# Kernel optimization log

Measured on AMD Instinct MI355X. Metric: run time of the kernel, lower is better.

## Reference

```python
import jax, jax.numpy as jnp
import numpy as np

MIN_DECAY = 0.8
N_SAMPLES = 32768
N_FRAMES = 128
D = 128
BATCH = 128
N_EVENTS = 8
START = 8      # ConvUpsample start size
SLOPE = 0.2    # leaky_relu negative slope


def _tconv(x, w, b):
    # ConvTranspose1d(kernel=4, stride=2, padding=1) -> doubles length.
    # Equivalent dilated conv needs explicit padding k-1-p = 2 per side.
    y = jax.lax.conv_transpose(x, w, strides=(2,), padding=[(2, 2)],
                               dimension_numbers=('NCH', 'IOH', 'NCH'))
    return y + b[None, :, None]


def setup_inputs() -> dict:
    key = jax.random.key(0)
    ks = jax.random.split(key, 16)
    s = 0.1  # weight_init
    inp = {
        'x': jax.random.normal(ks[0], (BATCH, N_EVENTS, D), jnp.float32),
        'noise': jax.random.uniform(ks[1], (BATCH * N_EVENTS, 1, N_SAMPLES), jnp.float32, -10.0, 10.0),
        'Wup': jax.random.normal(ks[2], (D, D * START), jnp.float32) * s,
        'bup': jnp.zeros((D * START,), jnp.float32),
    }
    for i in range(3):
        inp[f'Wd{i}'] = jax.random.normal(ks[3 + i], (D, D), jnp.float32) * s
        inp[f'bd{i}'] = jnp.zeros((D,), jnp.float32)
    inp['Wdo'] = jax.random.normal(ks[6], (D, 1), jnp.float32) * s
    inp['bdo'] = jnp.zeros((1,), jnp.float32)
    chans = [D, D, D, D, 1]  # frames: 8->16->32->64->128, last layer to 1 channel
    for i in range(4):
        inp[f'Wc{i}'] = jax.random.normal(ks[7 + i], (chans[i], chans[i + 1], 4), jnp.float32) * s
        inp[f'bc{i}'] = jnp.zeros((chans[i + 1],), jnp.float32)
    return inp


def reference(x, noise, Wup, bup, Wd0, bd0, Wd1, bd1, Wd2, bd2, Wdo, bdo,
              Wc0, bc0, Wc1, bc1, Wc2, bc2, Wc3, bc3):
    B, E, Dm = x.shape
    xf = x.reshape(-1, Dm)                      # [BE, D]
    # decay head: LinearOutputStack(D, 3, out_channels=1)
    h = xf
    for W, b in ((Wd0, bd0), (Wd1, bd1), (Wd2, bd2)):
        h = jax.nn.leaky_relu(h @ W + b, SLOPE)
    decay = MIN_DECAY + jax.nn.sigmoid(h @ Wdo + bdo) * (1.0 - MIN_DECAY)  # [BE, 1]
    # ConvUpsample('learned'): linear -> [BE, D, 8] -> 4 doubling tconvs -> [BE, 1, F]
    u = (xf @ Wup + bup).reshape(-1, Dm, START)
    u = jax.nn.leaky_relu(_tconv(u, Wc0, bc0), SLOPE)
    u = jax.nn.leaky_relu(_tconv(u, Wc1, bc1), SLOPE)
    u = jax.nn.leaky_relu(_tconv(u, Wc2, bc2), SLOPE)
    u = _tconv(u, Wc3, bc3)                     # [BE, 1, F]
    u = u ** 2
    # exponential-decay recurrence: v[i] = u[i] + decay * v[i-1]
    def step(carry, ut):
        v = ut + decay * carry
        return v, v
    seq = jnp.moveaxis(u, -1, 0)                # [F, BE, 1]
    _, vs = jax.lax.scan(step, jnp.zeros_like(seq[0]), seq)
    v = jnp.moveaxis(vs, 0, -1)                 # [BE, 1, F]
    # linear interpolation F -> N_SAMPLES (align_corners=False)
    pos = (jnp.arange(N_SAMPLES) + 0.5) * (N_FRAMES / N_SAMPLES) - 0.5
    pos = jnp.clip(pos, 0.0, N_FRAMES - 1)
    i0 = jnp.floor(pos).astype(jnp.int32)
    i1 = jnp.minimum(i0 + 1, N_FRAMES - 1)
    w = (pos - i0).astype(v.dtype)
    out = v[..., i0] * (1.0 - w) + v[..., i1] * w  # [BE, 1, N]
    out = out * noise
    return out.reshape(B, E, 1, N_SAMPLES)
```

## Files before the change

kernel.cpp:

```cpp
#include <hip/hip_runtime.h>

#define SLOPE 0.2f
__device__ __forceinline__ float lrelu(float v){ return v > 0.0f ? v : SLOPE*v; }

template<int LT, int LF, int IS, int OS, bool RELU>
__device__ __forceinline__ void tconv_tile(const float* __restrict__ W,
                                           const float* __restrict__ bias,
                                           const float* __restrict__ in,
                                           int base,
                                           float* __restrict__ out,
                                           int obase,
                                           int co, int q)
{
  constexpr int TQ = LT/2;
  constexpr int NI = LT/4;
  const int i0 = base + q*NI;
  float acc[TQ];
  {
    const float b = bias[co];
    #pragma unroll
    for (int j=0;j<TQ;j++) acc[j]=b;
  }
  const bool hasM1 = (i0 > 0);
  const bool hasE  = (i0 + NI < LF);
  #pragma unroll 2
  for (int ci=0; ci<128; ci++){
    const float4 w = *(const float4*)(W + ((size_t)ci*128 + co)*4);
    const float* xin = in + ci*IS + i0;
    const float xm1 = hasM1 ? xin[-1] : 0.0f;
    const float xE  = hasE  ? xin[NI] : 0.0f;
    float xv[NI];
    if constexpr (NI==2){ const float2 t=*(const float2*)xin; xv[0]=t.x; xv[1]=t.y; }
    else { const float4 t=*(const float4*)xin;
      xv[0]=t.x; xv[1]=t.y; xv[2]=t.z; xv[3]=t.w; }
    acc[0]    += xm1*w.x;
    acc[TQ-1] += xE *w.w;
    #pragma unroll
    for (int li=0; li<NI; li++){
      const float x = xv[li];
      acc[2*li]   += x*w.z;
      acc[2*li+1] += x*w.y;
      if (li<NI-1) acc[2*li+2] += x*w.x;
      if (li>0)    acc[2*li-1] += x*w.w;
    }
  }
  float* op = out + co*OS + obase + q*TQ;
  #pragma unroll
  for (int j=0;j<TQ;j++) op[j] = RELU ? lrelu(acc[j]) : acc[j];
}

__device__ __forceinline__ void final_tile(const float* __restrict__ Wc3,
                                           const float* __restrict__ bc3,
                                           const float* __restrict__ bufC,
                                           float* __restrict__ part,
                                           float* __restrict__ fr,
                                           int tt, int c, int g, int tid)
{
  const int off = tt*32;
  const int t = c;
  const bool inwin = (tt==0) ? (t < 63) : (t >= 63);
  const bool even = ((t & 1) == 0);
  const int i  = t >> 1;
  const int ia = even ? (i-1) : i;
  const int ib = even ? i : (i+1);
  const int sa = ia - off + 1;
  const int sbr = ib - off + 1;
  const float mb = (sbr <= 32) ? 1.0f : 0.0f;
  const int sb = (sbr <= 32) ? sbr : 32;
  float a = 0.0f;
  if (inwin){
    const int cb = g*32;
    #pragma unroll 4
    for (int k=0;k<32;k++){
      const int ci = cb + k;
      const float4 w = *(const float4*)(Wc3 + (size_t)ci*4);
      const float wa = even ? w.x : w.y;
      const float wb = even ? w.z : w.w;
      a += bufC[ci*33 + sa]*wa + (bufC[ci*33 + sb]*mb)*wb;
    }
  }
  part[g*128 + t] = a;
  __syncthreads();
  if (tid < 128 && ((tt==0) ? (tid < 63) : (tid >= 63))){
    const float s = part[tid]+part[128+tid]+part[256+tid]+part[384+tid] + bc3[0];
    fr[tid] = s*s;
  }
}

extern "C" __global__ __launch_bounds__(512, 8)
void npg_compute(const float* __restrict__ x,
                 const float* __restrict__ noise,
                 const float* __restrict__ Wup, const float* __restrict__ bup,
                 const float* __restrict__ Wd0, const float* __restrict__ bd0,
                 const float* __restrict__ Wd1, const float* __restrict__ bd1,
                 const float* __restrict__ Wd2, const float* __restrict__ bd2,
                 const float* __restrict__ Wdo, const float* __restrict__ bdo,
                 const float* __restrict__ Wc0, const float* __restrict__ bc0,
                 const float* __restrict__ Wc1, const float* __restrict__ bc1,
                 const float* __restrict__ Wc2, const float* __restrict__ bc2,
                 const float* __restrict__ Wc3, const float* __restrict__ bc3,
                 float* __restrict__ outp)
{
  __shared__ float R0[128*32];
  __shared__ float R1[128*33];
  __shared__ float part[512];
  __shared__ float fr[128];
  __shared__ float sdecay;

  float* const xrow = R1;
  float* const h0   = R1 + 128;
  float* const h1   = R1 + 256;

  const int tid = threadIdx.x;
  const int row = blockIdx.x;
  const int c   = tid & 127;
  const int g   = tid >> 7;

  if (tid < 128) xrow[tid] = x[row*128 + tid];
  __syncthreads();

  {
    const float* inb = xrow;
    const float* Ws[3] = {Wd0, Wd1, Wd2};
    const float* bs[3] = {bd0, bd1, bd2};
    float* outs[3] = {h0, h1, h0};
    #pragma unroll
    for (int layer=0; layer<3; layer++){
      float a = 0.0f;
      const int base = g*32;
      const float* W = Ws[layer];
      #pragma unroll 8
      for (int i=0;i<32;i++) a += inb[base+i]*W[(size_t)(base+i)*128 + c];
      part[g*128 + c] = a;
      __syncthreads();
      if (tid < 128){
        const float v = part[tid]+part[128+tid]+part[256+tid]+part[384+tid] + bs[layer][tid];
        outs[layer][tid] = lrelu(v);
      }
      __syncthreads();
      inb = outs[layer];
    }
    if (tid < 128) part[tid] = h0[tid]*Wdo[tid];
    __syncthreads();
    if (tid < 64){
      float v = part[tid] + part[tid+64];
      #pragma unroll
      for (int off=32; off>0; off>>=1) v += __shfl_down(v, off, 64);
      if (tid==0){
        const float z = v + bdo[0];
        sdecay = 0.8f + 0.2f/(1.0f + expf(-z));
      }
    }
    __syncthreads();
  }

  {
    const int o = tid*2;
    float2 a = make_float2(bup[o], bup[o+1]);
    #pragma unroll 4
    for (int i=0;i<128;i++){
      const float xv = xrow[i];
      const float2 w = *(const float2*)(Wup + (size_t)i*1024 + o);
      a.x += xv*w.x; a.y += xv*w.y;
    }
    R0[o] = a.x; R0[o+1] = a.y;
    __syncthreads();
  }

  tconv_tile<8 , 8, 8, 16, true>(Wc0, bc0, R0, 0, R1, 0, c, g);  __syncthreads();
  tconv_tile<16,16,16, 32, true>(Wc1, bc1, R1, 0, R0, 0, c, g);  __syncthreads();

  tconv_tile<16,32,32, 33, true>(Wc2, bc2, R0, 0, R1, 1, c, g);
  if (tid < 128) R1[tid*33] = 0.0f;
  __syncthreads();

  final_tile(Wc3, bc3, R1, part, fr, 0, c, g, tid);
  if (tid >= 128 && tid < 256){
    const int ci = tid - 128;
    R1[ci*33] = R1[ci*33 + 32];
  }
  __syncthreads();

  tconv_tile<16,32,32, 33, true>(Wc2, bc2, R0, 16, R1, 1, c, g);
  __syncthreads();

  final_tile(Wc3, bc3, R1, part, fr, 1, c, g, tid);
  __syncthreads();

  {
    float d = sdecay;
    #pragma unroll
    for (int o=1;o<128;o<<=1){
      const float prev = (tid < 128 && tid >= o) ? fr[tid-o] : 0.0f;
      __syncthreads();
      if (tid < 128) fr[tid] += d*prev;
      __syncthreads();
      d = d*d;
    }
  }

  {
    const float4* __restrict__ nz4 = (const float4*)(noise + (size_t)row*32768);
    float4*       __restrict__ o4  = (float4*)(outp  + (size_t)row*32768);
    #pragma unroll 8
    for (int it=0; it<16; ++it){
      const int idx = it*512 + tid;
      const float4 nz = nz4[idx];
      const int n = idx*4;
      float r[4];
      #pragma unroll
      for (int j=0;j<4;j++){
        float pos = ((float)(n+j) + 0.5f) * (1.0f/256.0f) - 0.5f;
        pos = fminf(fmaxf(pos, 0.0f), 127.0f);
        const int i0 = (int)pos;
        const int i1 = min(i0+1, 127);
        const float w = pos - (float)i0;
        r[j] = fr[i0]*(1.0f-w) + fr[i1]*w;
      }
      float4 o;
      o.x = r[0]*nz.x; o.y = r[1]*nz.y; o.z = r[2]*nz.z; o.w = r[3]*nz.w;
      o4[idx] = o;
    }
  }
}

extern "C" void kernel_launch(void* const* d_in, const int* in_sizes, int n_in,
                              void* d_out, int out_size, void* d_ws, size_t ws_size,
                              hipStream_t stream)
{
  const float* x    = (const float*)d_in[0];
  const float* noise= (const float*)d_in[1];
  const float* Wup  = (const float*)d_in[2];
  const float* bup  = (const float*)d_in[3];
  const float* Wd0  = (const float*)d_in[4];
  const float* bd0  = (const float*)d_in[5];
  const float* Wd1  = (const float*)d_in[6];
  const float* bd1  = (const float*)d_in[7];
  const float* Wd2  = (const float*)d_in[8];
  const float* bd2  = (const float*)d_in[9];
  const float* Wdo  = (const float*)d_in[10];
  const float* bdo  = (const float*)d_in[11];
  const float* Wc0  = (const float*)d_in[12];
  const float* bc0  = (const float*)d_in[13];
  const float* Wc1  = (const float*)d_in[14];
  const float* bc1  = (const float*)d_in[15];
  const float* Wc2  = (const float*)d_in[16];
  const float* bc2  = (const float*)d_in[17];
  const float* Wc3  = (const float*)d_in[18];
  const float* bc3  = (const float*)d_in[19];
  float* out = (float*)d_out;

  hipLaunchKernelGGL(npg_compute, dim3(1024), dim3(512), 0, stream,
                     x, noise, Wup, bup, Wd0, bd0, Wd1, bd1, Wd2, bd2, Wdo, bdo,
                     Wc0, bc0, Wc1, bc1, Wc2, bc2, Wc3, bc3, out);
}
```

Before: 465.1 us.

## Process two rows per block to reuse conv weights across rows

After: 452.5 us. 1.03x faster.

```diff
diff --git a/kernel.cpp b/kernel.cpp
--- a/kernel.cpp
+++ b/kernel.cpp
@@ -4,57 +4,65 @@
 __device__ __forceinline__ float lrelu(float v){ return v > 0.0f ? v : SLOPE*v; }
 
 template<int LT, int LF, int IS, int OS, bool RELU>
-__device__ __forceinline__ void tconv_tile(const float* __restrict__ W,
-                                           const float* __restrict__ bias,
-                                           const float* __restrict__ in,
-                                           int base,
-                                           float* __restrict__ out,
-                                           int obase,
-                                           int co, int q)
+__device__ __forceinline__ void tconv2r(const float* __restrict__ W,
+                                        const float* __restrict__ bias,
+                                        const float* __restrict__ in, int base,
+                                        float* __restrict__ out, int obase,
+                                        int co, int q)
 {
   constexpr int TQ = LT/2;
   constexpr int NI = LT/4;
   const int i0 = base + q*NI;
-  float acc[TQ];
+  float a0[TQ], a1[TQ];
   {
     const float b = bias[co];
     #pragma unroll
-    for (int j=0;j<TQ;j++) acc[j]=b;
+    for (int j=0;j<TQ;j++){ a0[j]=b; a1[j]=b; }
   }
   const bool hasM1 = (i0 > 0);
   const bool hasE  = (i0 + NI < LF);
   #pragma unroll 2
   for (int ci=0; ci<128; ci++){
     const float4 w = *(const float4*)(W + ((size_t)ci*128 + co)*4);
-    const float* xin = in + ci*IS + i0;
-    const float xm1 = hasM1 ? xin[-1] : 0.0f;
-    const float xE  = hasE  ? xin[NI] : 0.0f;
-    float xv[NI];
-    if constexpr (NI==2){ const float2 t=*(const float2*)xin; xv[0]=t.x; xv[1]=t.y; }
-    else { const float4 t=*(const float4*)xin;
-      xv[0]=t.x; xv[1]=t.y; xv[2]=t.z; xv[3]=t.w; }
-    acc[0]    += xm1*w.x;
-    acc[TQ-1] += xE *w.w;
+    const float* x0 = in + ci*(2*IS) + i0;
+    const float* x1 = x0 + IS;
+    const float xm10 = hasM1 ? x0[-1] : 0.0f;
+    const float xm11 = hasM1 ? x1[-1] : 0.0f;
+    const float xE0  = hasE  ? x0[NI] : 0.0f;
+    const float xE1  = hasE  ? x1[NI] : 0.0f;
+    float v0[NI], v1[NI];
+    if constexpr (NI==2){
+      const float2 t0=*(const float2*)x0; v0[0]=t0.x; v0[1]=t0.y;
+      const float2 t1=*(const float2*)x1; v1[0]=t1.x; v1[1]=t1.y;
+    } else {
+      const float4 t0=*(const float4*)x0; v0[0]=t0.x; v0[1]=t0.y; v0[2]=t0.z; v0[3]=t0.w;
+      const float4 t1=*(const float4*)x1; v1[0]=t1.x; v1[1]=t1.y; v1[2]=t1.z; v1[3]=t1.w;
+    }
+    a0[0]    += xm10*w.x;   a1[0]    += xm11*w.x;
+    a0[TQ-1] += xE0 *w.w;   a1[TQ-1] += xE1 *w.w;
     #pragma unroll
     for (int li=0; li<NI; li++){
-      const float x = xv[li];
-      acc[2*li]   += x*w.z;
-      acc[2*li+1] += x*w.y;
-      if (li<NI-1) acc[2*li+2] += x*w.x;
-      if (li>0)    acc[2*li-1] += x*w.w;
-    }
-  }
-  float* op = out + co*OS + obase + q*TQ;
+      a0[2*li]   += v0[li]*w.z;   a1[2*li]   += v1[li]*w.z;
+      a0[2*li+1] += v0[li]*w.y;   a1[2*li+1] += v1[li]*w.y;
+      if (li<NI-1){ a0[2*li+2] += v0[li]*w.x; a1[2*li+2] += v1[li]*w.x; }
+      if (li>0)   { a0[2*li-1] += v0[li]*w.w; a1[2*li-1] += v1[li]*w.w; }
+    }
+  }
+  float* op0 = out + co*(2*OS) + obase + q*TQ;
+  float* op1 = op0 + OS;
   #pragma unroll
-  for (int j=0;j<TQ;j++) op[j] = RELU ? lrelu(acc[j]) : acc[j];
-}
-
-__device__ __forceinline__ void final_tile(const float* __restrict__ Wc3,
-                                           const float* __restrict__ bc3,
-                                           const float* __restrict__ bufC,
-                                           float* __restrict__ part,
-                                           float* __restrict__ fr,
-                                           int tt, int c, int g, int tid)
+  for (int j=0;j<TQ;j++){
+    op0[j] = RELU ? lrelu(a0[j]) : a0[j];
+    op1[j] = RELU ? lrelu(a1[j]) : a1[j];
+  }
+}
+
+__device__ __forceinline__ void final2r(const float* __restrict__ Wc3,
+                                        const float* __restrict__ bc3,
+                                        const float* __restrict__ bufC,
+                                        float* __restrict__ part,
+                                        float* __restrict__ fr,
+                                        int tt, int c, int g, int tid)
 {
   const int off = tt*32;
   const int t = c;
@@ -67,7 +75,7 @@
   const int sbr = ib - off + 1;
   const float mb = (sbr <= 32) ? 1.0f : 0.0f;
   const int sb = (sbr <= 32) ? sbr : 32;
-  float a = 0.0f;
+  float A0 = 0.0f, A1 = 0.0f;
   if (inwin){
     const int cb = g*32;
     #pragma unroll 4
@@ -76,18 +84,26 @@
       const float4 w = *(const float4*)(Wc3 + (size_t)ci*4);
       const float wa = even ? w.x : w.y;
       const float wb = even ? w.z : w.w;
-      a += bufC[ci*33 + sa]*wa + (bufC[ci*33 + sb]*mb)*wb;
-    }
-  }
-  part[g*128 + t] = a;
-  __syncthreads();
-  if (tid < 128 && ((tt==0) ? (tid < 63) : (tid >= 63))){
-    const float s = part[tid]+part[128+tid]+part[256+tid]+part[384+tid] + bc3[0];
-    fr[tid] = s*s;
-  }
-}
-
-extern "C" __global__ __launch_bounds__(512, 8)
+      const float* bc = bufC + ci*66;
+      A0 += bc[sa]*wa + (bc[sb]*mb)*wb;
+      A1 += bc[33+sa]*wa + (bc[33+sb]*mb)*wb;
+    }
+  }
+  part[g*128 + t] = A0;
+  part[512 + g*128 + t] = A1;
+  __syncthreads();
+  if (tid < 256){
+    const int r = tid >> 7, t2 = tid & 127;
+    const bool w2 = (tt==0) ? (t2 < 63) : (t2 >= 63);
+    if (w2){
+      const float* p = part + r*512;
+      const float s = p[t2]+p[128+t2]+p[256+t2]+p[384+t2] + bc3[0];
+      fr[r*128 + t2] = s*s;
+    }
+  }
+}
+
+extern "C" __global__ __launch_bounds__(512, 4)
 void npg_compute(const float* __restrict__ x,
                  const float* __restrict__ noise,
                  const float* __restrict__ Wup, const float* __restrict__ bup,
@@ -101,54 +117,60 @@
                  const float* __restrict__ Wc3, const float* __restrict__ bc3,
                  float* __restrict__ outp)
 {
-  __shared__ float R0[128*32];
-  __shared__ float R1[128*33];
-  __shared__ float part[512];
-  __shared__ float fr[128];
-  __shared__ float sdecay;
-
-  float* const xrow = R1;
-  float* const h0   = R1 + 128;
-  float* const h1   = R1 + 256;
+  __shared__ float R0[128*64];
+  __shared__ float R1[128*66];
+  __shared__ float part[1024];
+  __shared__ float fr[256];
+  __shared__ float sdecay[2];
 
   const int tid = threadIdx.x;
-  const int row = blockIdx.x;
+  const int row0 = blockIdx.x * 2;
   const int c   = tid & 127;
   const int g   = tid >> 7;
 
-  if (tid < 128) xrow[tid] = x[row*128 + tid];
-  __syncthreads();
-
-  {
-    const float* inb = xrow;
+  if (tid < 256){
+    const int r = tid >> 7;
+    R1[tid] = x[(size_t)(row0 + r)*128 + (tid & 127)];
+  }
+  __syncthreads();
+
+  {
     const float* Ws[3] = {Wd0, Wd1, Wd2};
     const float* bs[3] = {bd0, bd1, bd2};
-    float* outs[3] = {h0, h1, h0};
+    const int inoff[4] = {0, 256, 512, 256};
+    const int r  = g >> 1;
+    const int gg = g & 1;
     #pragma unroll
     for (int layer=0; layer<3; layer++){
+      const float* inb = R1 + inoff[layer] + r*128;
       float a = 0.0f;
-      const int base = g*32;
+      const int base = gg*64;
       const float* W = Ws[layer];
       #pragma unroll 8
-      for (int i=0;i<32;i++) a += inb[base+i]*W[(size_t)(base+i)*128 + c];
+      for (int i=0;i<64;i++) a += inb[base+i]*W[(size_t)(base+i)*128 + c];
       part[g*128 + c] = a;
       __syncthreads();
-      if (tid < 128){
-        const float v = part[tid]+part[128+tid]+part[256+tid]+part[384+tid] + bs[layer][tid];
-        outs[layer][tid] = lrelu(v);
-      }
-      __syncthreads();
-      inb = outs[layer];
-    }
-    if (tid < 128) part[tid] = h0[tid]*Wdo[tid];
+      if (tid < 256){
+        const int rr = tid >> 7, t = tid & 127;
+        const float v = part[rr*256 + t] + part[rr*256 + 128 + t] + bs[layer][t];
+        R1[inoff[layer+1] + rr*128 + t] = lrelu(v);
+      }
+      __syncthreads();
+    }
+    if (tid < 256){
+      const int rr = tid >> 7, t = tid & 127;
+      part[tid] = R1[256 + rr*128 + t] * Wdo[t];
+    }
     __syncthreads();
-    if (tid < 64){
-      float v = part[tid] + part[tid+64];
+    if (tid < 128){
+      const int rr = tid >> 6;
+      const int lane = tid & 63;
+      float v = part[rr*128 + lane] + part[rr*128 + lane + 64];
       #pragma unroll
       for (int off=32; off>0; off>>=1) v += __shfl_down(v, off, 64);
-      if (tid==0){
+      if (lane == 0){
         const float z = v + bdo[0];
-        sdecay = 0.8f + 0.2f/(1.0f + expf(-z));
+        sdecay[rr] = 0.8f + 0.2f/(1.0f + expf(-z));
       }
     }
     __syncthreads();
@@ -156,70 +178,89 @@
 
   {
     const int o = tid*2;
-    float2 a = make_float2(bup[o], bup[o+1]);
+    const int co = o >> 3, s = o & 7;
+    float2 A0 = make_float2(bup[o], bup[o+1]);
+    float2 A1 = A0;
+    const float* x0 = R1;
+    const float* x1 = R1 + 128;
     #pragma unroll 4
     for (int i=0;i<128;i++){
-      const float xv = xrow[i];
       const float2 w = *(const float2*)(Wup + (size_t)i*1024 + o);
-      a.x += xv*w.x; a.y += xv*w.y;
-    }
-    R0[o] = a.x; R0[o+1] = a.y;
+      const float xv0 = x0[i], xv1 = x1[i];
+      A0.x += xv0*w.x; A0.y += xv0*w.y;
+      A1.x += xv1*w.x; A1.y += xv1*w.y;
+    }
+    float* d0 = R0 + co*16 + s;
+    d0[0] = A0.x; d0[1] = A0.y;
+    d0[8] = A1.x; d0[9] = A1.y;
     __syncthreads();
   }
 
-  tconv_tile<8 , 8, 8, 16, true>(Wc0, bc0, R0, 0, R1, 0, c, g);  __syncthreads();
-  tconv_tile<16,16,16, 32, true>(Wc1, bc1, R1, 0, R0, 0, c, g);  __syncthreads();
-
-  tconv_tile<16,32,32, 33, true>(Wc2, bc2, R0, 0, R1, 1, c, g);
-  if (tid < 128) R1[tid*33] = 0.0f;
-  __syncthreads();
-
-  final_tile(Wc3, bc3, R1, part, fr, 0, c, g, tid);
-  if (tid >= 128 && tid < 256){
-    const int ci = tid - 128;
-    R1[ci*33] = R1[ci*33 + 32];
-  }
-  __syncthreads();
-
-  tconv_tile<16,32,32, 33, true>(Wc2, bc2, R0, 16, R1, 1, c, g);
-  __syncthreads();
-
-  final_tile(Wc3, bc3, R1, part, fr, 1, c, g, tid);
-  __syncthreads();
-
-  {
-    float d = sdecay;
+  tconv2r<8 , 8, 8, 16, true>(Wc0, bc0, R0, 0, R1, 0, c, g);  __syncthreads();
+  tconv2r<16,16,16, 32, true>(Wc1, bc1, R1, 0, R0, 0, c, g);  __syncthreads();
+
+  tconv2r<16,32,32, 33, true>(Wc2, bc2, R0, 0, R1, 1, c, g);
+  if (tid < 256){ const int r = tid>>7, ci = tid&127; R1[ci*66 + r*33] = 0.0f; }
+  __syncthreads();
+
+  final2r(Wc3, bc3, R1, part, fr, 0, c, g, tid);
+  if (tid >= 256){
+    const int u = tid - 256;
+    const int r = u >> 7, ci = u & 127;
+    R1[ci*66 + r*33] = R1[ci*66 + r*33 + 32];
+  }
+  __syncthreads();
+
+  tconv2r<16,32,32, 33, true>(Wc2, bc2, R0, 16, R1, 1, c, g);
+  __syncthreads();
+
+  final2r(Wc3, bc3, R1, part, fr, 1, c, g, tid);
+  __syncthreads();
+
+  {
+    float d = (tid < 256) ? sdecay[tid >> 7] : 0.0f;
     #pragma unroll
     for (int o=1;o<128;o<<=1){
-      const float prev = (tid < 128 && tid >= o) ? fr[tid-o] : 0.0f;
-      __syncthreads();
-      if (tid < 128) fr[tid] += d*prev;
+      float prev = 0.0f;
+      if (tid < 256){
+        const int r = tid >> 7, t = tid & 127;
+        prev = (t >= o) ? fr[r*128 + t - o] : 0.0f;
+      }
+      __syncthreads();
+      if (tid < 256){
+        const int r = tid >> 7, t = tid & 127;
+        fr[r*128 + t] += d*prev;
+      }
       __syncthreads();
       d = d*d;
     }
   }
 
   {
-    const float4* __restrict__ nz4 = (const float4*)(noise + (size_t)row*32768);
-    float4*       __restrict__ o4  = (float4*)(outp  + (size_t)row*32768);
-    #pragma unroll 8
-    for (int it=0; it<16; ++it){
-      const int idx = it*512 + tid;
-      const float4 nz = nz4[idx];
-      const int n = idx*4;
-      float r[4];
-      #pragma unroll
-      for (int j=0;j<4;j++){
-        float pos = ((float)(n+j) + 0.5f) * (1.0f/256.0f) - 0.5f;
-        pos = fminf(fmaxf(pos, 0.0f), 127.0f);
-        const int i0 = (int)pos;
-        const int i1 = min(i0+1, 127);
-        const float w = pos - (float)i0;
-        r[j] = fr[i0]*(1.0f-w) + fr[i1]*w;
-      }
-      float4 o;
-      o.x = r[0]*nz.x; o.y = r[1]*nz.y; o.z = r[2]*nz.z; o.w = r[3]*nz.w;
-      o4[idx] = o;
+    #pragma unroll
+    for (int r=0;r<2;r++){
+      const float* frr = fr + r*128;
+      const float4* __restrict__ nz4 = (const float4*)(noise + (size_t)(row0+r)*32768);
+      float4*       __restrict__ o4  = (float4*)(outp  + (size_t)(row0+r)*32768);
+      #pragma unroll 4
+      for (int it=0; it<16; ++it){
+        const int idx = it*512 + tid;
+        const float4 nz = nz4[idx];
+        const int n = idx*4;
+        float rv[4];
+        #pragma unroll
+        for (int j=0;j<4;j++){
+          float pos = ((float)(n+j) + 0.5f) * (1.0f/256.0f) - 0.5f;
+          pos = fminf(fmaxf(pos, 0.0f), 127.0f);
+          const int i0 = (int)pos;
+          const int i1 = min(i0+1, 127);
+          const float w = pos - (float)i0;
+          rv[j] = frr[i0]*(1.0f-w) + frr[i1]*w;
+        }
+        float4 o;
+        o.x = rv[0]*nz.x; o.y = rv[1]*nz.y; o.z = rv[2]*nz.z; o.w = rv[3]*nz.w;
+        o4[idx] = o;
+      }
     }
   }
 }
@@ -250,7 +291,7 @@
   const float* bc3  = (const float*)d_in[19];
   float* out = (float*)d_out;
 
-  hipLaunchKernelGGL(npg_compute, dim3(1024), dim3(512), 0, stream,
+  hipLaunchKernelGGL(npg_compute, dim3(512), dim3(512), 0, stream,
                      x, noise, Wup, bup, Wd0, bd0, Wd1, bd1, Wd2, bd2, Wdo, bdo,
                      Wc0, bc0, Wc1, bc1, Wc2, bc2, Wc3, bc3, out);
 }
```
